# Kernel tuning notes

Hardware: AMD Instinct MI355X
Metric: run time of the kernel (lower is better)

## Reference

```python
import jax, jax.numpy as jnp
import numpy as np

PADDING = 4


def setup_inputs() -> dict:
    key = jax.random.key(0)
    k1, k2 = jax.random.split(key)
    n, c, h = 256, 12, 128
    x = jax.random.normal(k1, (n, c, h, h), dtype=jnp.float32)
    # integer pixel shift in [0, 2*padding], as torch.randint(0, 2*p+1, (n,1,1,2))
    shift = jax.random.randint(k2, (n, 1, 1, 2), 0, 2 * PADDING + 1, dtype=jnp.int32)
    return {"x": x, "shift": shift}


def _grid_sample_bilinear_zeros(x, grid):
    """x: [n,c,H,W], grid: [n,Ho,Wo,2] with (x,y) in [-1,1], align_corners=False,
    padding_mode='zeros'. Returns [n,c,Ho,Wo]."""
    n, c, H, W = x.shape
    Ho, Wo = grid.shape[1], grid.shape[2]
    # unnormalize (align_corners=False)
    ix = ((grid[..., 0] + 1.0) * W - 1.0) * 0.5  # [n,Ho,Wo]
    iy = ((grid[..., 1] + 1.0) * H - 1.0) * 0.5
    ix0 = jnp.floor(ix)
    iy0 = jnp.floor(iy)
    wx1 = ix - ix0
    wy1 = iy - iy0
    wx0 = 1.0 - wx1
    wy0 = 1.0 - wy1

    xf = x.reshape(n, c, H * W)

    def gather(iy_f, ix_f):
        valid = (ix_f >= 0) & (ix_f <= W - 1) & (iy_f >= 0) & (iy_f <= H - 1)
        iyc = jnp.clip(iy_f, 0, H - 1).astype(jnp.int32)
        ixc = jnp.clip(ix_f, 0, W - 1).astype(jnp.int32)
        idx = (iyc * W + ixc).reshape(n, 1, Ho * Wo)
        v = jnp.take_along_axis(xf, idx, axis=2).reshape(n, c, Ho, Wo)
        return v * valid.astype(x.dtype)[:, None]

    out = (gather(iy0, ix0) * (wy0 * wx0)[:, None]
           + gather(iy0, ix0 + 1.0) * (wy0 * wx1)[:, None]
           + gather(iy0 + 1.0, ix0) * (wy1 * wx0)[:, None]
           + gather(iy0 + 1.0, ix0 + 1.0) * (wy1 * wx1)[:, None])
    return out


def reference(x, shift):
    n, c, h, w = x.shape
    p = PADDING
    hp = h + 2 * p
    # replicate pad
    xp = jnp.pad(x, ((0, 0), (0, 0), (p, p), (p, p)), mode='edge')
    eps = 1.0 / hp
    arange = jnp.linspace(-1.0 + eps, 1.0 - eps, hp, dtype=x.dtype)[:h]  # [h]
    gx = jnp.broadcast_to(arange[None, :], (h, h))  # x coord varies along width
    gy = gx.T                                        # y coord varies along height
    base_grid = jnp.stack([gx, gy], axis=-1)[None]   # [1,h,h,2]
    grid = base_grid + shift.astype(x.dtype) * (2.0 / hp)  # [n,h,h,2]
    return _grid_sample_bilinear_zeros(xp, grid)
```

## Files before the change

kernel.cpp:

```cpp
#include <hip/hip_runtime.h>


constexpr int Himg = 128;
constexpr int Cimg = 12;
constexpr int PADc = 4;

__global__ __launch_bounds__(256) void random_shift_kernel(
    const float* __restrict__ x,
    const int* __restrict__ shift,
    float* __restrict__ out)
{
    const int n     = blockIdx.y;
    const int flat4 = blockIdx.x * 256 + threadIdx.x;
    const int col4  = flat4 & 31;
    const int rowi  = flat4 >> 5;
    const int j     = rowi & (Himg - 1);
    const int cc    = rowi >> 7;

    const int sx = shift[2 * n];
    const int sy = shift[2 * n + 1];
    const int dx = sx - PADc;
    const int dy = sy - PADc;

    int sj = j + dy;
    sj = sj < 0 ? 0 : (sj > Himg - 1 ? Himg - 1 : sj);

    const long long img_base = (long long)(n * Cimg + cc) * (Himg * Himg);
    const float* __restrict__ src_row = x + img_base + (long long)sj * Himg;
    float* __restrict__ dst = out + img_base + (long long)j * Himg + col4 * 4;

    const int i0 = col4 * 4 + dx;
    float4 v;
    if (i0 >= 0 && i0 + 3 <= Himg - 1) {
        v = *reinterpret_cast<const float4*>(src_row + i0);
    } else {
        int a = i0, b = i0 + 1, c2 = i0 + 2, d = i0 + 3;
        a  = a  < 0 ? 0 : (a  > Himg - 1 ? Himg - 1 : a);
        b  = b  < 0 ? 0 : (b  > Himg - 1 ? Himg - 1 : b);
        c2 = c2 < 0 ? 0 : (c2 > Himg - 1 ? Himg - 1 : c2);
        d  = d  < 0 ? 0 : (d  > Himg - 1 ? Himg - 1 : d);
        v = make_float4(src_row[a], src_row[b], src_row[c2], src_row[d]);
    }
    *reinterpret_cast<float4*>(dst) = v;
}

extern "C" void kernel_launch(void* const* d_in, const int* in_sizes, int n_in,
                              void* d_out, int out_size, void* d_ws, size_t ws_size,
                              hipStream_t stream) {
    const float* x     = (const float*)d_in[0];
    const int*   shift = (const int*)d_in[1];
    float*       out   = (float*)d_out;

    const int N = 256;
    dim3 grid(Cimg * Himg * (Himg / 4) / 256, N);
    random_shift_kernel<<<grid, 256, 0, stream>>>(x, shift, out);
}
```

Baseline: 316.9 us.

## Process whole plane per block with aligned vector loads and template shift dispatch

Each block now handles an entire 128x128 channel plane, with every thread looping over 16 rows instead of one float4 per thread. The horizontal shift is dispatched to a compile-time template, so unaligned reads become two aligned float4 loads plus register shuffles instead of scalar fallback loads. Stores are non-temporal and the shift values are made wave-uniform with readfirstlane. This cuts the grid size and per-thread setup, and avoids misaligned and scalar global accesses, at the cost of code size and fewer blocks in flight.

```diff
diff --git a/kernel.cpp b/kernel.cpp
--- a/kernel.cpp
+++ b/kernel.cpp
@@ -5,43 +5,92 @@
 constexpr int Cimg = 12;
 constexpr int PADc = 4;
 
+using f4 = __attribute__((ext_vector_type(4))) float;
+
+template <int DX>
+__device__ __forceinline__ void shift_plane(const float* __restrict__ src,
+                                            float* __restrict__ dstp,
+                                            int col4, int jrow0, int dy)
+{
+    if constexpr (DX == 0) {
+        const int q = col4 * 4;
+#pragma unroll
+        for (int it = 0; it < 16; ++it) {
+            const int j = jrow0 + it * 8;
+            int sj = j + dy; sj = sj < 0 ? 0 : (sj > Himg - 1 ? Himg - 1 : sj);
+            f4 v = *reinterpret_cast<const f4*>(src + sj * Himg + q);
+            __builtin_nontemporal_store(v, reinterpret_cast<f4*>(dstp + j * Himg));
+        }
+    } else {
+        constexpr int R = DX & 3;
+        const int q = col4 * 4 + (DX - R);
+        int qa = q;     if (qa < 0) qa = 0; if (qa > Himg - 4) qa = Himg - 4;
+        int qb = q + 4; if (qb < 0) qb = 0; if (qb > Himg - 4) qb = Himg - 4;
+        const bool edge = (DX > 0) ? (col4 == 31) : (col4 == 0);
+
+#define EIDX(e) (DX > 0 ? ((DX + (e)) > 3 ? 3 : (DX + (e))) \
+                        : ((DX + (e)) < 0 ? 0 : (DX + (e))))
+#pragma unroll
+        for (int it = 0; it < 16; ++it) {
+            const int j = jrow0 + it * 8;
+            int sj = j + dy; sj = sj < 0 ? 0 : (sj > Himg - 1 ? Himg - 1 : sj);
+            const float* row = src + sj * Himg;
+            const f4 A = *reinterpret_cast<const f4*>(row + qa);
+            f4 vi;
+            if constexpr (R != 0) {
+                const f4 B = *reinterpret_cast<const f4*>(row + qb);
+                vi[0] = (R + 0 < 4) ? A[(R + 0) & 3] : B[(R + 0) & 3];
+                vi[1] = (R + 1 < 4) ? A[(R + 1) & 3] : B[(R + 1) & 3];
+                vi[2] = (R + 2 < 4) ? A[(R + 2) & 3] : B[(R + 2) & 3];
+                vi[3] = (R + 3 < 4) ? A[(R + 3) & 3] : B[(R + 3) & 3];
+            } else {
+                vi = A;
+            }
+            f4 ve;
+            ve[0] = A[EIDX(0)]; ve[1] = A[EIDX(1)];
+            ve[2] = A[EIDX(2)]; ve[3] = A[EIDX(3)];
+            f4 v;
+            v[0] = edge ? ve[0] : vi[0];
+            v[1] = edge ? ve[1] : vi[1];
+            v[2] = edge ? ve[2] : vi[2];
+            v[3] = edge ? ve[3] : vi[3];
+            __builtin_nontemporal_store(v, reinterpret_cast<f4*>(dstp + j * Himg));
+        }
+#undef EIDX
+    }
+}
+
 __global__ __launch_bounds__(256) void random_shift_kernel(
     const float* __restrict__ x,
     const int* __restrict__ shift,
     float* __restrict__ out)
 {
-    const int n     = blockIdx.y;
-    const int flat4 = blockIdx.x * 256 + threadIdx.x;
-    const int col4  = flat4 & 31;
-    const int rowi  = flat4 >> 5;
-    const int j     = rowi & (Himg - 1);
-    const int cc    = rowi >> 7;
+    const int cc  = blockIdx.x;
+    const int n   = blockIdx.y;
+    const int tid = threadIdx.x;
+    const int col4  = tid & 31;
+    const int jrow0 = tid >> 5;
 
-    const int sx = shift[2 * n];
-    const int sy = shift[2 * n + 1];
+    const int sx = __builtin_amdgcn_readfirstlane(shift[2 * n]);
+    const int sy = __builtin_amdgcn_readfirstlane(shift[2 * n + 1]);
     const int dx = sx - PADc;
     const int dy = sy - PADc;
 
-    int sj = j + dy;
-    sj = sj < 0 ? 0 : (sj > Himg - 1 ? Himg - 1 : sj);
+    const size_t plane = (size_t)(n * Cimg + cc) * (Himg * Himg);
+    const float* __restrict__ src  = x   + plane;
+    float* __restrict__       dstp = out + plane + col4 * 4;
 
-    const long long img_base = (long long)(n * Cimg + cc) * (Himg * Himg);
-    const float* __restrict__ src_row = x + img_base + (long long)sj * Himg;
-    float* __restrict__ dst = out + img_base + (long long)j * Himg + col4 * 4;
-
-    const int i0 = col4 * 4 + dx;
-    float4 v;
-    if (i0 >= 0 && i0 + 3 <= Himg - 1) {
-        v = *reinterpret_cast<const float4*>(src_row + i0);
-    } else {
-        int a = i0, b = i0 + 1, c2 = i0 + 2, d = i0 + 3;
-        a  = a  < 0 ? 0 : (a  > Himg - 1 ? Himg - 1 : a);
-        b  = b  < 0 ? 0 : (b  > Himg - 1 ? Himg - 1 : b);
-        c2 = c2 < 0 ? 0 : (c2 > Himg - 1 ? Himg - 1 : c2);
-        d  = d  < 0 ? 0 : (d  > Himg - 1 ? Himg - 1 : d);
-        v = make_float4(src_row[a], src_row[b], src_row[c2], src_row[d]);
+    switch (dx) {
+        case -4: shift_plane<-4>(src, dstp, col4, jrow0, dy); break;
+        case -3: shift_plane<-3>(src, dstp, col4, jrow0, dy); break;
+        case -2: shift_plane<-2>(src, dstp, col4, jrow0, dy); break;
+        case -1: shift_plane<-1>(src, dstp, col4, jrow0, dy); break;
+        case  0: shift_plane< 0>(src, dstp, col4, jrow0, dy); break;
+        case  1: shift_plane< 1>(src, dstp, col4, jrow0, dy); break;
+        case  2: shift_plane< 2>(src, dstp, col4, jrow0, dy); break;
+        case  3: shift_plane< 3>(src, dstp, col4, jrow0, dy); break;
+        default: shift_plane< 4>(src, dstp, col4, jrow0, dy); break;
     }
-    *reinterpret_cast<float4*>(dst) = v;
 }
 
 extern "C" void kernel_launch(void* const* d_in, const int* in_sizes, int n_in,
@@ -51,7 +100,6 @@
     const int*   shift = (const int*)d_in[1];
     float*       out   = (float*)d_out;
 
-    const int N = 256;
-    dim3 grid(Cimg * Himg * (Himg / 4) / 256, N);
+    dim3 grid(Cimg, 256);
     random_shift_kernel<<<grid, 256, 0, stream>>>(x, shift, out);
 }
```

New measurement: 348.4 us. 9.9% more time.
